# Performance work log

Hardware: AMD Instinct MI355X
Metric: run time of the kernel (lower is better)

Reference implementation:

```python
import jax, jax.numpy as jnp
import numpy as np

N_NODES = 100000
N_EDGES = 1600000
N_GRAPHS = 256
F_IN = 128
HID = 128


def gcn_conv(x, W, b, src, dst, n_nodes):
    """PyG GCNConv: h = D^{-1/2}(A+I)D^{-1/2} (x @ W) + b, self-loops added."""
    h = x @ W  # [N, H]
    ones = jnp.ones((src.shape[0],), dtype=x.dtype)
    deg = jax.ops.segment_sum(ones, dst, num_segments=n_nodes) + 1.0  # +1 self-loop
    dinv = jax.lax.rsqrt(deg)  # deg >= 1 always
    norm = dinv[src] * dinv[dst]  # [E]
    msgs = h[src] * norm[:, None]  # gather + scale, [E, H]
    agg = jax.ops.segment_sum(msgs, dst, num_segments=n_nodes)  # scatter-add
    agg = agg + h * (dinv * dinv)[:, None]  # self-loop contribution
    return agg + b


def setup_inputs() -> dict:
    key = jax.random.key(0)
    ks = jax.random.split(key, 8)
    x = jax.random.normal(ks[0], (N_NODES, F_IN), dtype=jnp.float32)
    edge_index = jax.random.randint(ks[1], (2, N_EDGES), 0, N_NODES, dtype=jnp.int64)
    batch = jnp.sort(jax.random.randint(ks[2], (N_NODES,), 0, N_GRAPHS, dtype=jnp.int64))
    s1 = 1.0 / np.sqrt(F_IN)
    s2 = 1.0 / np.sqrt(HID)
    w1 = jax.random.normal(ks[3], (F_IN, HID), dtype=jnp.float32) * s1
    b1 = jnp.zeros((HID,), dtype=jnp.float32)
    w2 = jax.random.normal(ks[4], (HID, HID), dtype=jnp.float32) * s2
    b2 = jnp.zeros((HID,), dtype=jnp.float32)
    w_out = jax.random.normal(ks[5], (HID, 1), dtype=jnp.float32) * s2
    b_out = jnp.zeros((1,), dtype=jnp.float32)
    return {"x": x, "edge_index": edge_index, "batch": batch,
            "w1": w1, "b1": b1, "w2": w2, "b2": b2,
            "w_out": w_out, "b_out": b_out}


def reference(x, edge_index, batch, w1, b1, w2, b2, w_out, b_out):
    src, dst = edge_index[0], edge_index[1]
    n = x.shape[0]
    h = jax.nn.relu(gcn_conv(x, w1, b1, src, dst, n))
    h = jax.nn.relu(gcn_conv(h, w2, b2, src, dst, n))
    # global mean pool over graphs
    sums = jax.ops.segment_sum(h, batch, num_segments=N_GRAPHS)  # [G, H]
    counts = jax.ops.segment_sum(jnp.ones((n,), dtype=h.dtype), batch, num_segments=N_GRAPHS)
    pooled = sums / jnp.maximum(counts, 1.0)[:, None]
    return pooled @ w_out + b_out  # [G, 1]
```

## Files before the change

### kernel.cpp

```cpp
#include <hip/hip_runtime.h>
#include <hip/hip_fp16.h>

#define N_NODES 100000
#define N_EDGES 1600000
#define N_GRAPHS 256
#define NB 1563
#define BCAP 1280
#define SBLOCKS 128

typedef _Float16 half8 __attribute__((ext_vector_type(8)));
typedef float f32x4 __attribute__((ext_vector_type(4)));

__device__ __forceinline__ unsigned pack2(float a, float b) {
    __half2 h = __floats2half2_rn(a, b);
    return *reinterpret_cast<unsigned*>(&h);
}

__global__ __launch_bounds__(1024) void stage_kernel(const int* __restrict__ src,
                                                     const int* __restrict__ dst,
                                                     int* __restrict__ bucket_cur,
                                                     unsigned* __restrict__ pairbuf) {
    __shared__ int lcnt[NB];
    __shared__ int lcur[NB];
    const int tid = threadIdx.x;
    const int per = (N_EDGES + SBLOCKS - 1) / SBLOCKS;
    const int e0 = blockIdx.x * per;
    const int e1 = min(e0 + per, N_EDGES);

    for (int i = tid; i < NB; i += 1024) lcnt[i] = 0;
    __syncthreads();
    for (int e = e0 + tid; e < e1; e += 1024)
        atomicAdd(&lcnt[dst[e] >> 6], 1);
    __syncthreads();
    for (int i = tid; i < NB; i += 1024) {
        int c = lcnt[i];
        lcur[i] = c ? atomicAdd(&bucket_cur[i], c) : 0;
    }
    __syncthreads();
    for (int e = e0 + tid; e < e1; e += 1024) {
        int d = dst[e];
        int b = d >> 6;
        int p = atomicAdd(&lcur[b], 1);
        if (p < BCAP)
            pairbuf[(size_t)b * BCAP + p] =
                ((unsigned)(d & 63) << 17) | (unsigned)src[e];
    }
}

#define BVPT 7
__global__ __launch_bounds__(256) void scan_buckets_kernel(const int* __restrict__ bucket_cur,
                                                           int* __restrict__ bucket_off) {
    __shared__ int tsum[256];
    int tid = threadIdx.x;
    int v[BVPT];
    int s = 0;
#pragma unroll
    for (int j = 0; j < BVPT; ++j) {
        int idx = tid * BVPT + j;
        v[j] = (idx < NB) ? min(bucket_cur[idx], BCAP) : 0;
        s += v[j];
    }
    tsum[tid] = s;
    __syncthreads();
    for (int off = 1; off < 256; off <<= 1) {
        int y = (tid >= off) ? tsum[tid - off] : 0;
        __syncthreads();
        tsum[tid] += y;
        __syncthreads();
    }
    int run = (tid > 0) ? tsum[tid - 1] : 0;
#pragma unroll
    for (int j = 0; j < BVPT; ++j) {
        int idx = tid * BVPT + j;
        if (idx < NB) bucket_off[idx] = run;
        run += v[j];
    }
    if (tid == 255) bucket_off[NB] = tsum[255];
}

__global__ __launch_bounds__(256) void localsort_kernel(const unsigned* __restrict__ pairbuf,
                                                        const int* __restrict__ bucket_cur,
                                                        const int* __restrict__ bucket_off,
                                                        int* __restrict__ csr_src,
                                                        int* __restrict__ row_off,
                                                        float* __restrict__ dinv) {
    __shared__ int ldeg[64];
    __shared__ int loff[64];
    __shared__ int lcur[64];
    int tid = threadIdx.x;
    int b = blockIdx.x;
    int cnt = min(bucket_cur[b], BCAP);
    int base = bucket_off[b];
    const unsigned* pb = pairbuf + (size_t)b * BCAP;
    int n0 = b << 6;

    if (tid < 64) ldeg[tid] = 0;
    __syncthreads();
    for (int i = tid; i < cnt; i += 256)
        atomicAdd(&ldeg[pb[i] >> 17], 1);
    __syncthreads();
    if (tid < 64) loff[tid] = ldeg[tid];
    __syncthreads();
    for (int off = 1; off < 64; off <<= 1) {
        int y = 0;
        if (tid < 64 && tid >= off) y = loff[tid - off];
        __syncthreads();
        if (tid < 64) loff[tid] += y;
        __syncthreads();
    }
    if (tid < 64) {
        int ex = loff[tid] - ldeg[tid];
        lcur[tid] = ex;
        int n = n0 + tid;
        if (n < N_NODES) {
            row_off[n] = base + ex;
            dinv[n] = rsqrtf((float)ldeg[tid] + 1.0f);
        }
    }
    __syncthreads();
    for (int i = tid; i < cnt; i += 256) {
        unsigned w = pb[i];
        int dl = w >> 17;
        int s = (int)(w & 0x1FFFFu);
        int p = atomicAdd(&lcur[dl], 1);
        csr_src[base + p] = s;
    }
}

__global__ __launch_bounds__(256) void wprep_kernel(const float* __restrict__ W,
                                                    __half* __restrict__ Wt) {
    int t = blockIdx.x * 256 + threadIdx.x;
    int n = t >> 7, k = t & 127;
    Wt[t] = (__half)W[k * 128 + n];
}

__global__ __launch_bounds__(256) void gemm_mfma_kernel(const float* __restrict__ Xf,
                                                        const __half* __restrict__ Xh,
                                                        const __half* __restrict__ Wt,
                                                        const float* __restrict__ dinv,
                                                        __half* __restrict__ HT,
                                                        int xf16) {
    __shared__ __half Xl[128][136];
    __shared__ __half Wl[128][136];
    const int tid = threadIdx.x;
    const int row0 = blockIdx.x * 128;

#pragma unroll
    for (int i = 0; i < 8; ++i) {
        int idx = tid + i * 256;
        int n = idx >> 4, c0 = (idx & 15) * 8;
        *(uint4*)&Wl[n][c0] = *(const uint4*)&Wt[n * 128 + c0];
    }
    if (xf16) {
#pragma unroll
        for (int i = 0; i < 8; ++i) {
            int idx = tid + i * 256;
            int r = idx >> 4, c0 = (idx & 15) * 8;
            int rr = min(row0 + r, N_NODES - 1);
            *(uint4*)&Xl[r][c0] = *(const uint4*)&Xh[(size_t)rr * 128 + c0];
        }
    } else {
#pragma unroll
        for (int i = 0; i < 16; ++i) {
            int idx = tid + i * 256;
            int r = idx >> 5, c0 = (idx & 31) * 4;
            int rr = min(row0 + r, N_NODES - 1);
            float4 v = *(const float4*)&Xf[(size_t)rr * 128 + c0];
            uint2 o;
            o.x = pack2(v.x, v.y);
            o.y = pack2(v.z, v.w);
            *(uint2*)&Xl[r][c0] = o;
        }
    }
    __syncthreads();

    const int wv = tid >> 6;
    const int lane = tid & 63;
    const int lr = lane & 15;
    const int lg = lane >> 4;

    f32x4 acc[2][8];
#pragma unroll
    for (int mt = 0; mt < 2; ++mt)
#pragma unroll
        for (int nt = 0; nt < 8; ++nt) acc[mt][nt] = (f32x4){0.f, 0.f, 0.f, 0.f};

#pragma unroll
    for (int ks = 0; ks < 4; ++ks) {
        const int kb = ks * 32 + lg * 8;
        half8 a0 = *reinterpret_cast<const half8*>(&Xl[wv * 32 + lr][kb]);
        half8 a1 = *reinterpret_cast<const half8*>(&Xl[wv * 32 + 16 + lr][kb]);
        half8 b[8];
#pragma unroll
        for (int nt = 0; nt < 8; ++nt)
            b[nt] = *reinterpret_cast<const half8*>(&Wl[nt * 16 + lr][kb]);
#pragma unroll
        for (int nt = 0; nt < 8; ++nt) {
            acc[0][nt] = __builtin_amdgcn_mfma_f32_16x16x32_f16(a0, b[nt], acc[0][nt], 0, 0, 0);
            acc[1][nt] = __builtin_amdgcn_mfma_f32_16x16x32_f16(a1, b[nt], acc[1][nt], 0, 0, 0);
        }
    }

#pragma unroll
    for (int mt = 0; mt < 2; ++mt) {
#pragma unroll
        for (int i = 0; i < 4; ++i) {
            int rr = row0 + wv * 32 + mt * 16 + lg * 4 + i;
            if (rr < N_NODES) {
                float di = dinv[rr];
#pragma unroll
                for (int nt = 0; nt < 8; ++nt)
                    HT[(size_t)rr * 128 + nt * 16 + lr] = (__half)(acc[mt][nt][i] * di);
            }
        }
    }
}

__device__ __forceinline__ void add8(float* a, uint4 w) {
    float2 p0 = __half22float2(*reinterpret_cast<__half2*>(&w.x));
    float2 p1 = __half22float2(*reinterpret_cast<__half2*>(&w.y));
    float2 p2 = __half22float2(*reinterpret_cast<__half2*>(&w.z));
    float2 p3 = __half22float2(*reinterpret_cast<__half2*>(&w.w));
    a[0] += p0.x; a[1] += p0.y; a[2] += p1.x; a[3] += p1.y;
    a[4] += p2.x; a[5] += p2.y; a[6] += p3.x; a[7] += p3.y;
}
__global__ __launch_bounds__(256) void gather_kernel(const int* __restrict__ row_off,
                                                     const int* __restrict__ csr_src,
                                                     const __half* __restrict__ ht,
                                                     const float* __restrict__ dinv,
                                                     const float* __restrict__ b,
                                                     __half* __restrict__ Y) {
    int t = blockIdx.x * 256 + threadIdx.x;
    int n = t >> 4;
    if (n >= N_NODES) return;
    int f = (t & 15) * 8;
    int e0 = row_off[n];
    int e1 = (n < N_NODES - 1) ? row_off[n + 1] : N_EDGES;
    const __half* htf = ht + f;

    float a0[8] = {0,0,0,0,0,0,0,0};
    float a1[8] = {0,0,0,0,0,0,0,0};
    float a2[8] = {0,0,0,0,0,0,0,0};
    float a3[8] = {0,0,0,0,0,0,0,0};
    add8(a0, *(const uint4*)&htf[(size_t)n * 128]);

    int e = e0;
    for (; e + 4 <= e1; e += 4) {
        int s0 = csr_src[e], s1 = csr_src[e + 1];
        int s2 = csr_src[e + 2], s3 = csr_src[e + 3];
        uint4 w0 = *(const uint4*)&htf[(size_t)s0 * 128];
        uint4 w1 = *(const uint4*)&htf[(size_t)s1 * 128];
        uint4 w2 = *(const uint4*)&htf[(size_t)s2 * 128];
        uint4 w3 = *(const uint4*)&htf[(size_t)s3 * 128];
        add8(a0, w0); add8(a1, w1); add8(a2, w2); add8(a3, w3);
    }
    for (; e < e1; ++e)
        add8(a0, *(const uint4*)&htf[(size_t)csr_src[e] * 128]);

    float di = dinv[n];
    float4 bb0 = *(const float4*)&b[f];
    float4 bb1 = *(const float4*)&b[f + 4];
    float r0 = fmaxf((a0[0]+a1[0]+a2[0]+a3[0]) * di + bb0.x, 0.0f);
    float r1 = fmaxf((a0[1]+a1[1]+a2[1]+a3[1]) * di + bb0.y, 0.0f);
    float r2 = fmaxf((a0[2]+a1[2]+a2[2]+a3[2]) * di + bb0.z, 0.0f);
    float r3 = fmaxf((a0[3]+a1[3]+a2[3]+a3[3]) * di + bb0.w, 0.0f);
    float r4 = fmaxf((a0[4]+a1[4]+a2[4]+a3[4]) * di + bb1.x, 0.0f);
    float r5 = fmaxf((a0[5]+a1[5]+a2[5]+a3[5]) * di + bb1.y, 0.0f);
    float r6 = fmaxf((a0[6]+a1[6]+a2[6]+a3[6]) * di + bb1.z, 0.0f);
    float r7 = fmaxf((a0[7]+a1[7]+a2[7]+a3[7]) * di + bb1.w, 0.0f);
    uint4 o;
    o.x = pack2(r0, r1);
    o.y = pack2(r2, r3);
    o.z = pack2(r4, r5);
    o.w = pack2(r6, r7);
    *(uint4*)&Y[(size_t)n * 128 + f] = o;
}

#define NODES_PER_GROUP 100
__global__ __launch_bounds__(256) void pool_kernel(const __half* __restrict__ Y,
                                                   const int* __restrict__ batch,
                                                   float* __restrict__ pooled,
                                                   float* __restrict__ counts) {
    int g = (blockIdx.x * 256 + threadIdx.x) >> 5;
    int lane = threadIdx.x & 31;
    int f = lane * 4;
    int n0 = g * NODES_PER_GROUP;
    if (n0 >= N_NODES) return;
    int n1 = min(n0 + NODES_PER_GROUP, N_NODES);
    int cur = batch[n0];
    float4 acc = make_float4(0, 0, 0, 0);
    float cnt = 0.0f;
    for (int n = n0; n < n1; ++n) {
        int bid = batch[n];
        if (bid != cur) {
            float* p = &pooled[cur * 128 + f];
            atomicAdd(p + 0, acc.x); atomicAdd(p + 1, acc.y);
            atomicAdd(p + 2, acc.z); atomicAdd(p + 3, acc.w);
            if (lane == 0) atomicAdd(&counts[cur], cnt);
            acc = make_float4(0, 0, 0, 0); cnt = 0.0f; cur = bid;
        }
        uint2 w = *(const uint2*)&Y[(size_t)n * 128 + f];
        float2 p0 = __half22float2(*reinterpret_cast<__half2*>(&w.x));
        float2 p1 = __half22float2(*reinterpret_cast<__half2*>(&w.y));
        acc.x += p0.x; acc.y += p0.y; acc.z += p1.x; acc.w += p1.y;
        cnt += 1.0f;
    }
    float* p = &pooled[cur * 128 + f];
    atomicAdd(p + 0, acc.x); atomicAdd(p + 1, acc.y);
    atomicAdd(p + 2, acc.z); atomicAdd(p + 3, acc.w);
    if (lane == 0) atomicAdd(&counts[cur], cnt);
}

__global__ __launch_bounds__(256) void out_kernel(const float* __restrict__ pooled,
                                                  const float* __restrict__ counts,
                                                  const float* __restrict__ w_out,
                                                  const float* __restrict__ b_out,
                                                  float* __restrict__ out) {
    int gph = threadIdx.x;
    float c = fmaxf(counts[gph], 1.0f);
    float s = 0.0f;
    for (int f = 0; f < 128; ++f) s += pooled[gph * 128 + f] * w_out[f];
    out[gph] = s / c + b_out[0];
}

extern "C" void kernel_launch(void* const* d_in, const int* in_sizes, int n_in,
                              void* d_out, int out_size, void* d_ws, size_t ws_size,
                              hipStream_t stream) {
    const float* x     = (const float*)d_in[0];
    const int*   edge  = (const int*)d_in[1];
    const int*   batch = (const int*)d_in[2];
    const float* w1    = (const float*)d_in[3];
    const float* b1    = (const float*)d_in[4];
    const float* w2    = (const float*)d_in[5];
    const float* b2    = (const float*)d_in[6];
    const float* w_out = (const float*)d_in[7];
    const float* b_out = (const float*)d_in[8];
    float* out = (float*)d_out;

    char* ws = (char*)d_ws;
    size_t off = 0;
    auto alloc = [&](size_t bytes) {
        void* p = ws + off;
        off += (bytes + 511) & ~(size_t)511;
        return p;
    };
    const size_t FEAT_BYTES = (size_t)N_NODES * 128 * 4;
    __half*   ht16       = (__half*)alloc(FEAT_BYTES / 2);
    __half*   y16        = (__half*)alloc(FEAT_BYTES / 2);
    unsigned* pairbuf    = (unsigned*)y16;
    float*    dinv       = (float*)alloc(N_NODES * 4);
    int*      row_off    = (int*)alloc(N_NODES * 4);
    int*      csr_src    = (int*)alloc(N_EDGES * 4);
    int*      bucket_cur = (int*)alloc((NB + 1) * 4);
    int*      bucket_off = (int*)alloc((NB + 1) * 4);
    __half*   wt1        = (__half*)alloc(128 * 128 * 2);
    __half*   wt2        = (__half*)alloc(128 * 128 * 2);
    float*    pooled     = (float*)alloc(N_GRAPHS * 128 * 4);
    float*    counts     = (float*)alloc(N_GRAPHS * 4);

    const int* src = edge;
    const int* dst = edge + N_EDGES;

    hipMemsetAsync(bucket_cur, 0, (NB + 1) * 4, stream);
    hipMemsetAsync(pooled, 0, N_GRAPHS * 128 * 4, stream);
    hipMemsetAsync(counts, 0, N_GRAPHS * 4, stream);

    wprep_kernel<<<64, 256, 0, stream>>>(w1, wt1);
    wprep_kernel<<<64, 256, 0, stream>>>(w2, wt2);

    stage_kernel<<<SBLOCKS, 1024, 0, stream>>>(src, dst, bucket_cur, pairbuf);
    scan_buckets_kernel<<<1, 256, 0, stream>>>(bucket_cur, bucket_off);
    localsort_kernel<<<NB, 256, 0, stream>>>(pairbuf, bucket_cur, bucket_off,
                                             csr_src, row_off, dinv);

    int gblocks = (N_NODES + 127) / 128;
    gemm_mfma_kernel<<<gblocks, 256, 0, stream>>>(x, (const __half*)nullptr, wt1, dinv, ht16, 0);
    gather_kernel<<<(N_NODES * 16 + 255) / 256, 256, 0, stream>>>(row_off, csr_src, ht16, dinv, b1, y16);

    gemm_mfma_kernel<<<gblocks, 256, 0, stream>>>((const float*)nullptr, y16, wt2, dinv, ht16, 1);
    gather_kernel<<<(N_NODES * 16 + 255) / 256, 256, 0, stream>>>(row_off, csr_src, ht16, dinv, b2, y16);

    int ngroups = (N_NODES + NODES_PER_GROUP - 1) / NODES_PER_GROUP;
    pool_kernel<<<(ngroups * 32 + 255) / 256, 256, 0, stream>>>(y16, batch, pooled, counts);
    out_kernel<<<1, 256, 0, stream>>>(pooled, counts, w_out, b_out, out);
}
```

Before: 263.4 us.

## Co-schedule histogram with first GEMM, exact-count CSR scatter, fused pool/output

```diff
diff --git a/kernel.cpp b/kernel.cpp
--- a/kernel.cpp
+++ b/kernel.cpp
@@ -5,8 +5,8 @@
 #define N_EDGES 1600000
 #define N_GRAPHS 256
 #define NB 1563
-#define BCAP 1280
-#define SBLOCKS 128
+#define SBLOCKS 256
+#define GB1 782
 
 typedef _Float16 half8 __attribute__((ext_vector_type(8)));
 typedef float f32x4 __attribute__((ext_vector_type(4)));
@@ -16,40 +16,152 @@
     return *reinterpret_cast<unsigned*>(&h);
 }
 
-__global__ __launch_bounds__(1024) void stage_kernel(const int* __restrict__ src,
-                                                     const int* __restrict__ dst,
-                                                     int* __restrict__ bucket_cur,
-                                                     unsigned* __restrict__ pairbuf) {
-    __shared__ int lcnt[NB];
-    __shared__ int lcur[NB];
+__global__ __launch_bounds__(256) void wprep_kernel(const float* __restrict__ W1,
+                                                    const float* __restrict__ W2,
+                                                    __half* __restrict__ Wt1,
+                                                    __half* __restrict__ Wt2) {
+    int b = blockIdx.x;
+    const float* W = (b < 64) ? W1 : W2;
+    __half* Wt = (b < 64) ? Wt1 : Wt2;
+    int t = (b & 63) * 256 + threadIdx.x;
+    int n = t >> 7, k = t & 127;
+    Wt[t] = (__half)W[k * 128 + n];
+}
+
+__global__ __launch_bounds__(256) void gemmhist_kernel(const float* __restrict__ Xf,
+                                                       const __half* __restrict__ Xh,
+                                                       const __half* __restrict__ Wt,
+                                                       const float* __restrict__ dinv,
+                                                       __half* __restrict__ HT,
+                                                       int xf16, int withDinv,
+                                                       const int* __restrict__ dst,
+                                                       int* __restrict__ cnt2d,
+                                                       int histBlocks) {
+    __shared__ __align__(16) char smem[69632];
     const int tid = threadIdx.x;
-    const int per = (N_EDGES + SBLOCKS - 1) / SBLOCKS;
-    const int e0 = blockIdx.x * per;
-    const int e1 = min(e0 + per, N_EDGES);
-
-    for (int i = tid; i < NB; i += 1024) lcnt[i] = 0;
-    __syncthreads();
-    for (int e = e0 + tid; e < e1; e += 1024)
-        atomicAdd(&lcnt[dst[e] >> 6], 1);
-    __syncthreads();
-    for (int i = tid; i < NB; i += 1024) {
-        int c = lcnt[i];
-        lcur[i] = c ? atomicAdd(&bucket_cur[i], c) : 0;
-    }
-    __syncthreads();
-    for (int e = e0 + tid; e < e1; e += 1024) {
-        int d = dst[e];
-        int b = d >> 6;
-        int p = atomicAdd(&lcur[b], 1);
-        if (p < BCAP)
-            pairbuf[(size_t)b * BCAP + p] =
-                ((unsigned)(d & 63) << 17) | (unsigned)src[e];
-    }
+    int bid = blockIdx.x;
+    bool isHist = false;
+    int id = bid;
+    if (histBlocks) {
+        if (bid < 1024) {
+            if ((bid & 3) == 0) { isHist = true; id = bid >> 2; }
+            else id = (bid >> 2) * 3 + (bid & 3) - 1;
+        } else {
+            id = 768 + (bid - 1024);
+        }
+    }
+
+    if (isHist) {
+        int* lcnt = (int*)smem;
+        for (int i = tid; i < NB; i += 256) lcnt[i] = 0;
+        __syncthreads();
+        const int per = (N_EDGES + SBLOCKS - 1) / SBLOCKS;
+        int e0 = id * per, e1 = min(e0 + per, N_EDGES);
+        for (int e = e0 + tid; e < e1; e += 256)
+            atomicAdd(&lcnt[dst[e] >> 6], 1);
+        __syncthreads();
+        for (int i = tid; i < NB; i += 256)
+            cnt2d[id * NB + i] = lcnt[i];
+        return;
+    }
+
+    typedef __half (*TileT)[136];
+    TileT Xl = (TileT)smem;
+    TileT Wl = (TileT)(smem + 34816);
+    const int row0 = id * 128;
+
+#pragma unroll
+    for (int i = 0; i < 8; ++i) {
+        int idx = tid + i * 256;
+        int n = idx >> 4, c0 = (idx & 15) * 8;
+        *(uint4*)&Wl[n][c0] = *(const uint4*)&Wt[n * 128 + c0];
+    }
+    if (xf16) {
+#pragma unroll
+        for (int i = 0; i < 8; ++i) {
+            int idx = tid + i * 256;
+            int r = idx >> 4, c0 = (idx & 15) * 8;
+            int rr = min(row0 + r, N_NODES - 1);
+            *(uint4*)&Xl[r][c0] = *(const uint4*)&Xh[(size_t)rr * 128 + c0];
+        }
+    } else {
+#pragma unroll
+        for (int i = 0; i < 16; ++i) {
+            int idx = tid + i * 256;
+            int r = idx >> 5, c0 = (idx & 31) * 4;
+            int rr = min(row0 + r, N_NODES - 1);
+            float4 v = *(const float4*)&Xf[(size_t)rr * 128 + c0];
+            uint2 o;
+            o.x = pack2(v.x, v.y);
+            o.y = pack2(v.z, v.w);
+            *(uint2*)&Xl[r][c0] = o;
+        }
+    }
+    __syncthreads();
+
+    const int wv = tid >> 6;
+    const int lane = tid & 63;
+    const int lr = lane & 15;
+    const int lg = lane >> 4;
+
+    f32x4 acc[2][8];
+#pragma unroll
+    for (int mt = 0; mt < 2; ++mt)
+#pragma unroll
+        for (int nt = 0; nt < 8; ++nt) acc[mt][nt] = (f32x4){0.f, 0.f, 0.f, 0.f};
+
+#pragma unroll
+    for (int ks = 0; ks < 4; ++ks) {
+        const int kb = ks * 32 + lg * 8;
+        half8 a0 = *reinterpret_cast<const half8*>(&Xl[wv * 32 + lr][kb]);
+        half8 a1 = *reinterpret_cast<const half8*>(&Xl[wv * 32 + 16 + lr][kb]);
+        half8 b[8];
+#pragma unroll
+        for (int nt = 0; nt < 8; ++nt)
+            b[nt] = *reinterpret_cast<const half8*>(&Wl[nt * 16 + lr][kb]);
+#pragma unroll
+        for (int nt = 0; nt < 8; ++nt) {
+            acc[0][nt] = __builtin_amdgcn_mfma_f32_16x16x32_f16(a0, b[nt], acc[0][nt], 0, 0, 0);
+            acc[1][nt] = __builtin_amdgcn_mfma_f32_16x16x32_f16(a1, b[nt], acc[1][nt], 0, 0, 0);
+        }
+    }
+
+#pragma unroll
+    for (int mt = 0; mt < 2; ++mt) {
+#pragma unroll
+        for (int i = 0; i < 4; ++i) {
+            int rr = row0 + wv * 32 + mt * 16 + lg * 4 + i;
+            if (rr < N_NODES) {
+                float di = withDinv ? dinv[rr] : 1.0f;
+#pragma unroll
+                for (int nt = 0; nt < 8; ++nt)
+                    HT[(size_t)rr * 128 + nt * 16 + lr] = (__half)(acc[mt][nt][i] * di);
+            }
+        }
+    }
+}
+
+__global__ __launch_bounds__(256) void scan2d_kernel(int* __restrict__ cnt2d,
+                                                     int* __restrict__ bucket_cnt) {
+    __shared__ int ts[256];
+    int i = blockIdx.x;
+    int t = threadIdx.x;
+    int v = cnt2d[t * NB + i];
+    ts[t] = v;
+    __syncthreads();
+    for (int off = 1; off < 256; off <<= 1) {
+        int y = (t >= off) ? ts[t - off] : 0;
+        __syncthreads();
+        ts[t] += y;
+        __syncthreads();
+    }
+    cnt2d[t * NB + i] = ts[t] - v;
+    if (t == 255) bucket_cnt[i] = ts[255];
 }
 
 #define BVPT 7
-__global__ __launch_bounds__(256) void scan_buckets_kernel(const int* __restrict__ bucket_cur,
-                                                           int* __restrict__ bucket_off) {
+__global__ __launch_bounds__(256) void scanB_kernel(const int* __restrict__ bucket_cnt,
+                                                    int* __restrict__ bucket_off) {
     __shared__ int tsum[256];
     int tid = threadIdx.x;
     int v[BVPT];
@@ -57,7 +169,7 @@
 #pragma unroll
     for (int j = 0; j < BVPT; ++j) {
         int idx = tid * BVPT + j;
-        v[j] = (idx < NB) ? min(bucket_cur[idx], BCAP) : 0;
+        v[j] = (idx < NB) ? bucket_cnt[idx] : 0;
         s += v[j];
     }
     tsum[tid] = s;
@@ -78,8 +190,28 @@
     if (tid == 255) bucket_off[NB] = tsum[255];
 }
 
+__global__ __launch_bounds__(256) void scatter_kernel(const int* __restrict__ src,
+                                                      const int* __restrict__ dst,
+                                                      const int* __restrict__ cnt2d,
+                                                      const int* __restrict__ bucket_off,
+                                                      unsigned* __restrict__ pairbuf) {
+    __shared__ int lcur[NB];
+    const int tid = threadIdx.x;
+    const int blk = blockIdx.x;
+    for (int i = tid; i < NB; i += 256)
+        lcur[i] = bucket_off[i] + cnt2d[blk * NB + i];
+    __syncthreads();
+    const int per = (N_EDGES + SBLOCKS - 1) / SBLOCKS;
+    int e0 = blk * per, e1 = min(e0 + per, N_EDGES);
+    for (int e = e0 + tid; e < e1; e += 256) {
+        int d = dst[e];
+        int b = d >> 6;
+        int p = atomicAdd(&lcur[b], 1);
+        pairbuf[p] = ((unsigned)(d & 63) << 17) | (unsigned)src[e];
+    }
+}
+
 __global__ __launch_bounds__(256) void localsort_kernel(const unsigned* __restrict__ pairbuf,
-                                                        const int* __restrict__ bucket_cur,
                                                         const int* __restrict__ bucket_off,
                                                         int* __restrict__ csr_src,
                                                         int* __restrict__ row_off,
@@ -89,9 +221,9 @@
     __shared__ int lcur[64];
     int tid = threadIdx.x;
     int b = blockIdx.x;
-    int cnt = min(bucket_cur[b], BCAP);
     int base = bucket_off[b];
-    const unsigned* pb = pairbuf + (size_t)b * BCAP;
+    int cnt = bucket_off[b + 1] - base;
+    const unsigned* pb = pairbuf + base;
     int n0 = b << 6;
 
     if (tid < 64) ldeg[tid] = 0;
@@ -127,95 +259,6 @@
     }
 }
 
-__global__ __launch_bounds__(256) void wprep_kernel(const float* __restrict__ W,
-                                                    __half* __restrict__ Wt) {
-    int t = blockIdx.x * 256 + threadIdx.x;
-    int n = t >> 7, k = t & 127;
-    Wt[t] = (__half)W[k * 128 + n];
-}
-
-__global__ __launch_bounds__(256) void gemm_mfma_kernel(const float* __restrict__ Xf,
-                                                        const __half* __restrict__ Xh,
-                                                        const __half* __restrict__ Wt,
-                                                        const float* __restrict__ dinv,
-                                                        __half* __restrict__ HT,
-                                                        int xf16) {
-    __shared__ __half Xl[128][136];
-    __shared__ __half Wl[128][136];
-    const int tid = threadIdx.x;
-    const int row0 = blockIdx.x * 128;
-
-#pragma unroll
-    for (int i = 0; i < 8; ++i) {
-        int idx = tid + i * 256;
-        int n = idx >> 4, c0 = (idx & 15) * 8;
-        *(uint4*)&Wl[n][c0] = *(const uint4*)&Wt[n * 128 + c0];
-    }
-    if (xf16) {
-#pragma unroll
-        for (int i = 0; i < 8; ++i) {
-            int idx = tid + i * 256;
-            int r = idx >> 4, c0 = (idx & 15) * 8;
-            int rr = min(row0 + r, N_NODES - 1);
-            *(uint4*)&Xl[r][c0] = *(const uint4*)&Xh[(size_t)rr * 128 + c0];
-        }
-    } else {
-#pragma unroll
-        for (int i = 0; i < 16; ++i) {
-            int idx = tid + i * 256;
-            int r = idx >> 5, c0 = (idx & 31) * 4;
-            int rr = min(row0 + r, N_NODES - 1);
-            float4 v = *(const float4*)&Xf[(size_t)rr * 128 + c0];
-            uint2 o;
-            o.x = pack2(v.x, v.y);
-            o.y = pack2(v.z, v.w);
-            *(uint2*)&Xl[r][c0] = o;
-        }
-    }
-    __syncthreads();
-
-    const int wv = tid >> 6;
-    const int lane = tid & 63;
-    const int lr = lane & 15;
-    const int lg = lane >> 4;
-
-    f32x4 acc[2][8];
-#pragma unroll
-    for (int mt = 0; mt < 2; ++mt)
-#pragma unroll
-        for (int nt = 0; nt < 8; ++nt) acc[mt][nt] = (f32x4){0.f, 0.f, 0.f, 0.f};
-
-#pragma unroll
-    for (int ks = 0; ks < 4; ++ks) {
-        const int kb = ks * 32 + lg * 8;
-        half8 a0 = *reinterpret_cast<const half8*>(&Xl[wv * 32 + lr][kb]);
-        half8 a1 = *reinterpret_cast<const half8*>(&Xl[wv * 32 + 16 + lr][kb]);
-        half8 b[8];
-#pragma unroll
-        for (int nt = 0; nt < 8; ++nt)
-            b[nt] = *reinterpret_cast<const half8*>(&Wl[nt * 16 + lr][kb]);
-#pragma unroll
-        for (int nt = 0; nt < 8; ++nt) {
-            acc[0][nt] = __builtin_amdgcn_mfma_f32_16x16x32_f16(a0, b[nt], acc[0][nt], 0, 0, 0);
-            acc[1][nt] = __builtin_amdgcn_mfma_f32_16x16x32_f16(a1, b[nt], acc[1][nt], 0, 0, 0);
-        }
-    }
-
-#pragma unroll
-    for (int mt = 0; mt < 2; ++mt) {
-#pragma unroll
-        for (int i = 0; i < 4; ++i) {
-            int rr = row0 + wv * 32 + mt * 16 + lg * 4 + i;
-            if (rr < N_NODES) {
-                float di = dinv[rr];
-#pragma unroll
-                for (int nt = 0; nt < 8; ++nt)
-                    HT[(size_t)rr * 128 + nt * 16 + lr] = (__half)(acc[mt][nt][i] * di);
-            }
-        }
-    }
-}
-
 __device__ __forceinline__ void add8(float* a, uint4 w) {
     float2 p0 = __half22float2(*reinterpret_cast<__half2*>(&w.x));
     float2 p1 = __half22float2(*reinterpret_cast<__half2*>(&w.y));
@@ -224,11 +267,22 @@
     a[0] += p0.x; a[1] += p0.y; a[2] += p1.x; a[3] += p1.y;
     a[4] += p2.x; a[5] += p2.y; a[6] += p3.x; a[7] += p3.y;
 }
+__device__ __forceinline__ void fma8(float* a, uint4 w, float s) {
+    float2 p0 = __half22float2(*reinterpret_cast<__half2*>(&w.x));
+    float2 p1 = __half22float2(*reinterpret_cast<__half2*>(&w.y));
+    float2 p2 = __half22float2(*reinterpret_cast<__half2*>(&w.z));
+    float2 p3 = __half22float2(*reinterpret_cast<__half2*>(&w.w));
+    a[0] = fmaf(s, p0.x, a[0]); a[1] = fmaf(s, p0.y, a[1]);
+    a[2] = fmaf(s, p1.x, a[2]); a[3] = fmaf(s, p1.y, a[3]);
+    a[4] = fmaf(s, p2.x, a[4]); a[5] = fmaf(s, p2.y, a[5]);
+    a[6] = fmaf(s, p3.x, a[6]); a[7] = fmaf(s, p3.y, a[7]);
+}
+template<bool DV>
 __global__ __launch_bounds__(256) void gather_kernel(const int* __restrict__ row_off,
                                                      const int* __restrict__ csr_src,
                                                      const __half* __restrict__ ht,
                                                      const float* __restrict__ dinv,
-                                                     const float* __restrict__ b,
+                                                     const float* __restrict__ bias,
                                                      __half* __restrict__ Y) {
     int t = blockIdx.x * 256 + threadIdx.x;
     int n = t >> 4;
@@ -237,13 +291,16 @@
     int e0 = row_off[n];
     int e1 = (n < N_NODES - 1) ? row_off[n + 1] : N_EDGES;
     const __half* htf = ht + f;
+    float dn = dinv[n];
 
     float a0[8] = {0,0,0,0,0,0,0,0};
     float a1[8] = {0,0,0,0,0,0,0,0};
     float a2[8] = {0,0,0,0,0,0,0,0};
     float a3[8] = {0,0,0,0,0,0,0,0};
-    add8(a0, *(const uint4*)&htf[(size_t)n * 128]);
-
+    {
+        uint4 w = *(const uint4*)&htf[(size_t)n * 128];
+        if (DV) fma8(a0, w, dn); else add8(a0, w);
+    }
     int e = e0;
     for (; e + 4 <= e1; e += 4) {
         int s0 = csr_src[e], s1 = csr_src[e + 1];
@@ -252,22 +309,29 @@
         uint4 w1 = *(const uint4*)&htf[(size_t)s1 * 128];
         uint4 w2 = *(const uint4*)&htf[(size_t)s2 * 128];
         uint4 w3 = *(const uint4*)&htf[(size_t)s3 * 128];
-        add8(a0, w0); add8(a1, w1); add8(a2, w2); add8(a3, w3);
-    }
-    for (; e < e1; ++e)
-        add8(a0, *(const uint4*)&htf[(size_t)csr_src[e] * 128]);
-
-    float di = dinv[n];
-    float4 bb0 = *(const float4*)&b[f];
-    float4 bb1 = *(const float4*)&b[f + 4];
-    float r0 = fmaxf((a0[0]+a1[0]+a2[0]+a3[0]) * di + bb0.x, 0.0f);
-    float r1 = fmaxf((a0[1]+a1[1]+a2[1]+a3[1]) * di + bb0.y, 0.0f);
-    float r2 = fmaxf((a0[2]+a1[2]+a2[2]+a3[2]) * di + bb0.z, 0.0f);
-    float r3 = fmaxf((a0[3]+a1[3]+a2[3]+a3[3]) * di + bb0.w, 0.0f);
-    float r4 = fmaxf((a0[4]+a1[4]+a2[4]+a3[4]) * di + bb1.x, 0.0f);
-    float r5 = fmaxf((a0[5]+a1[5]+a2[5]+a3[5]) * di + bb1.y, 0.0f);
-    float r6 = fmaxf((a0[6]+a1[6]+a2[6]+a3[6]) * di + bb1.z, 0.0f);
-    float r7 = fmaxf((a0[7]+a1[7]+a2[7]+a3[7]) * di + bb1.w, 0.0f);
+        if (DV) {
+            fma8(a0, w0, dinv[s0]); fma8(a1, w1, dinv[s1]);
+            fma8(a2, w2, dinv[s2]); fma8(a3, w3, dinv[s3]);
+        } else {
+            add8(a0, w0); add8(a1, w1); add8(a2, w2); add8(a3, w3);
+        }
+    }
+    for (; e < e1; ++e) {
+        int s = csr_src[e];
+        uint4 w = *(const uint4*)&htf[(size_t)s * 128];
+        if (DV) fma8(a0, w, dinv[s]); else add8(a0, w);
+    }
+
+    float4 bb0 = *(const float4*)&bias[f];
+    float4 bb1 = *(const float4*)&bias[f + 4];
+    float r0 = fmaxf((a0[0]+a1[0]+a2[0]+a3[0]) * dn + bb0.x, 0.0f);
+    float r1 = fmaxf((a0[1]+a1[1]+a2[1]+a3[1]) * dn + bb0.y, 0.0f);
+    float r2 = fmaxf((a0[2]+a1[2]+a2[2]+a3[2]) * dn + bb0.z, 0.0f);
+    float r3 = fmaxf((a0[3]+a1[3]+a2[3]+a3[3]) * dn + bb0.w, 0.0f);
+    float r4 = fmaxf((a0[4]+a1[4]+a2[4]+a3[4]) * dn + bb1.x, 0.0f);
+    float r5 = fmaxf((a0[5]+a1[5]+a2[5]+a3[5]) * dn + bb1.y, 0.0f);
+    float r6 = fmaxf((a0[6]+a1[6]+a2[6]+a3[6]) * dn + bb1.z, 0.0f);
+    float r7 = fmaxf((a0[7]+a1[7]+a2[7]+a3[7]) * dn + bb1.w, 0.0f);
     uint4 o;
     o.x = pack2(r0, r1);
     o.y = pack2(r2, r3);
@@ -276,51 +340,45 @@
     *(uint4*)&Y[(size_t)n * 128 + f] = o;
 }
 
-#define NODES_PER_GROUP 100
-__global__ __launch_bounds__(256) void pool_kernel(const __half* __restrict__ Y,
-                                                   const int* __restrict__ batch,
-                                                   float* __restrict__ pooled,
-                                                   float* __restrict__ counts) {
-    int g = (blockIdx.x * 256 + threadIdx.x) >> 5;
-    int lane = threadIdx.x & 31;
-    int f = lane * 4;
-    int n0 = g * NODES_PER_GROUP;
-    if (n0 >= N_NODES) return;
-    int n1 = min(n0 + NODES_PER_GROUP, N_NODES);
-    int cur = batch[n0];
+__global__ __launch_bounds__(256) void poolout_kernel(const __half* __restrict__ Y,
+                                                      const int* __restrict__ batch,
+                                                      const float* __restrict__ w_out,
+                                                      const float* __restrict__ b_out,
+                                                      float* __restrict__ out) {
+    __shared__ float red[8][128];
+    __shared__ float pr[128];
+    int g = blockIdx.x;
+    int tid = threadIdx.x;
+    int lo = 0, hi = N_NODES;
+    while (lo < hi) { int m = (lo + hi) >> 1; if (batch[m] < g) lo = m + 1; else hi = m; }
+    int lo2 = lo, hi2 = N_NODES;
+    while (lo2 < hi2) { int m = (lo2 + hi2) >> 1; if (batch[m] < g + 1) lo2 = m + 1; else hi2 = m; }
+    int cnt = lo2 - lo;
+
+    int rslot = tid >> 5;
+    int f = (tid & 31) * 4;
     float4 acc = make_float4(0, 0, 0, 0);
-    float cnt = 0.0f;
-    for (int n = n0; n < n1; ++n) {
-        int bid = batch[n];
-        if (bid != cur) {
-            float* p = &pooled[cur * 128 + f];
-            atomicAdd(p + 0, acc.x); atomicAdd(p + 1, acc.y);
-            atomicAdd(p + 2, acc.z); atomicAdd(p + 3, acc.w);
-            if (lane == 0) atomicAdd(&counts[cur], cnt);
-            acc = make_float4(0, 0, 0, 0); cnt = 0.0f; cur = bid;
-        }
+    for (int n = lo + rslot; n < lo2; n += 8) {
         uint2 w = *(const uint2*)&Y[(size_t)n * 128 + f];
         float2 p0 = __half22float2(*reinterpret_cast<__half2*>(&w.x));
         float2 p1 = __half22float2(*reinterpret_cast<__half2*>(&w.y));
         acc.x += p0.x; acc.y += p0.y; acc.z += p1.x; acc.w += p1.y;
-        cnt += 1.0f;
-    }
-    float* p = &pooled[cur * 128 + f];
-    atomicAdd(p + 0, acc.x); atomicAdd(p + 1, acc.y);
-    atomicAdd(p + 2, acc.z); atomicAdd(p + 3, acc.w);
-    if (lane == 0) atomicAdd(&counts[cur], cnt);
-}
-
-__global__ __launch_bounds__(256) void out_kernel(const float* __restrict__ pooled,
-                                                  const float* __restrict__ counts,
-                                                  const float* __restrict__ w_out,
-                                                  const float* __restrict__ b_out,
-                                                  float* __restrict__ out) {
-    int gph = threadIdx.x;
-    float c = fmaxf(counts[gph], 1.0f);
-    float s = 0.0f;
-    for (int f = 0; f < 128; ++f) s += pooled[gph * 128 + f] * w_out[f];
-    out[gph] = s / c + b_out[0];
+    }
+    *(float4*)&red[rslot][f] = acc;
+    __syncthreads();
+    if (tid < 128) {
+        float s = 0.0f;
+#pragma unroll
+        for (int r = 0; r < 8; ++r) s += red[r][tid];
+        pr[tid] = s * w_out[tid];
+    }
+    __syncthreads();
+    for (int off = 64; off >= 1; off >>= 1) {
+        if (tid < off) pr[tid] += pr[tid + off];
+        __syncthreads();
+    }
+    if (tid == 0)
+        out[g] = pr[0] / fmaxf((float)cnt, 1.0f) + b_out[0];
 }
 
 extern "C" void kernel_launch(void* const* d_in, const int* in_sizes, int n_in,
@@ -351,36 +409,34 @@
     float*    dinv       = (float*)alloc(N_NODES * 4);
     int*      row_off    = (int*)alloc(N_NODES * 4);
     int*      csr_src    = (int*)alloc(N_EDGES * 4);
-    int*      bucket_cur = (int*)alloc((NB + 1) * 4);
+    int*      cnt2d      = (int*)alloc((size_t)SBLOCKS * NB * 4);
+    int*      bucket_cnt = (int*)alloc((NB + 1) * 4);
     int*      bucket_off = (int*)alloc((NB + 1) * 4);
     __half*   wt1        = (__half*)alloc(128 * 128 * 2);
     __half*   wt2        = (__half*)alloc(128 * 128 * 2);
-    float*    pooled     = (float*)alloc(N_GRAPHS * 128 * 4);
-    float*    counts     = (float*)alloc(N_GRAPHS * 4);
 
     const int* src = edge;
     const int* dst = edge + N_EDGES;
 
-    hipMemsetAsync(bucket_cur, 0, (NB + 1) * 4, stream);
-    hipMemsetAsync(pooled, 0, N_GRAPHS * 128 * 4, stream);
-    hipMemsetAsync(counts, 0, N_GRAPHS * 4, stream);
-
-    wprep_kernel<<<64, 256, 0, stream>>>(w1, wt1);
-    wprep_kernel<<<64, 256, 0, stream>>>(w2, wt2);
-
-    stage_kernel<<<SBLOCKS, 1024, 0, stream>>>(src, dst, bucket_cur, pairbuf);
-    scan_buckets_kernel<<<1, 256, 0, stream>>>(bucket_cur, bucket_off);
-    localsort_kernel<<<NB, 256, 0, stream>>>(pairbuf, bucket_cur, bucket_off,
-                                             csr_src, row_off, dinv);
-
-    int gblocks = (N_NODES + 127) / 128;
-    gemm_mfma_kernel<<<gblocks, 256, 0, stream>>>(x, (const __half*)nullptr, wt1, dinv, ht16, 0);
-    gather_kernel<<<(N_NODES * 16 + 255) / 256, 256, 0, stream>>>(row_off, csr_src, ht16, dinv, b1, y16);
-
-    gemm_mfma_kernel<<<gblocks, 256, 0, stream>>>((const float*)nullptr, y16, wt2, dinv, ht16, 1);
-    gather_kernel<<<(N_NODES * 16 + 255) / 256, 256, 0, stream>>>(row_off, csr_src, ht16, dinv, b2, y16);
-
-    int ngroups = (N_NODES + NODES_PER_GROUP - 1) / NODES_PER_GROUP;
-    pool_kernel<<<(ngroups * 32 + 255) / 256, 256, 0, stream>>>(y16, batch, pooled, counts);
-    out_kernel<<<1, 256, 0, stream>>>(pooled, counts, w_out, b_out, out);
-}
+    wprep_kernel<<<128, 256, 0, stream>>>(w1, w2, wt1, wt2);
+
+    gemmhist_kernel<<<1024 + (GB1 - 768), 256, 0, stream>>>(
+        x, (const __half*)nullptr, wt1, (const float*)nullptr, ht16,
+        0, 0, dst, cnt2d, 1);
+
+    scan2d_kernel<<<NB, 256, 0, stream>>>(cnt2d, bucket_cnt);
+    scanB_kernel<<<1, 256, 0, stream>>>(bucket_cnt, bucket_off);
+    scatter_kernel<<<SBLOCKS, 256, 0, stream>>>(src, dst, cnt2d, bucket_off, pairbuf);
+    localsort_kernel<<<NB, 256, 0, stream>>>(pairbuf, bucket_off, csr_src, row_off, dinv);
+
+    gather_kernel<true><<<(N_NODES * 16 + 255) / 256, 256, 0, stream>>>(
+        row_off, csr_src, ht16, dinv, b1, y16);
+
+    gemmhist_kernel<<<GB1, 256, 0, stream>>>(
+        (const float*)nullptr, y16, wt2, dinv, ht16, 1, 1,
+        (const int*)nullptr, (int*)nullptr, 0);
+    gather_kernel<false><<<(N_NODES * 16 + 255) / 256, 256, 0, stream>>>(
+        row_off, csr_src, ht16, dinv, b2, y16);
+
+    poolout_kernel<<<N_GRAPHS, 256, 0, stream>>>(y16, batch, w_out, b_out, out);
+}
```

After: 236.0 us. 10.4% less time.
